# Optimization experiments

Hardware: AMD Instinct MI355X
Metric: run time of the kernel (lower is better)

The kernel has to match this reference:

```python
import jax, jax.numpy as jnp
import numpy as np

S = 8192          # tokens
D = 4096          # model_dim
E = 64            # num_experts
CAP_FACTOR = 1.0
MIN_CAPACITY = 8
CAPACITY = max(int(np.ceil(S / E * CAP_FACTOR)), MIN_CAPACITY)  # = 128


def setup_inputs() -> dict:
    key = jax.random.key(0)
    kx, kw = jax.random.split(key)
    x = jax.random.normal(kx, (S, D), dtype=jnp.float32)
    # torch Linear weight [out_features, in_features] = [E, D]
    wg = jax.random.normal(kw, (E, D), dtype=jnp.float32) * (1.0 / np.sqrt(D))
    return {"x": x, "wg": wg}


def reference(x, wg):
    # logits = wg(input_fp32): [s, e]
    logits = jnp.einsum('sd,ed->se', x.astype(jnp.float32), wg)
    gates = jax.nn.softmax(logits, axis=1)                     # [s, e]

    # top-1 expert per token (argmax of softmax == argmax of logits)
    indices1_s = jnp.argmax(gates, axis=1)                     # [s]
    mask1 = jax.nn.one_hot(indices1_s, E, dtype=jnp.int32)     # [s, e]
    exp_counts = jnp.sum(mask1, axis=0)                        # [e]

    # load-balancing aux loss (uses pre-capacity mask, as in torch)
    me = jnp.mean(gates, axis=0)
    ce = jnp.mean(mask1.astype(jnp.float32), axis=0)
    l_aux = jnp.sum(me * ce) * E

    # capacity truncation: keep first CAPACITY routed tokens per expert
    # (equivalent to mask1 * scatter(topk(mask1, capacity, dim=0)) when
    #  use_rts=False, since topk over 0/1 tie-breaks by lowest index)
    loc0 = jnp.cumsum(mask1, axis=0) - 1                       # [s, e]
    mask1 = mask1 * (loc0 < CAPACITY).astype(jnp.int32)

    # slot positions within each expert's capacity buffer
    locations1 = jnp.cumsum(mask1, axis=0) - 1                 # [s, e]
    locations1_s = jnp.sum(locations1 * mask1, axis=1)         # [s]

    mask1_float = mask1.astype(jnp.float32)
    gates = gates * mask1_float                                # [s, e]
    locations1_sc = jax.nn.one_hot(locations1_s, CAPACITY, dtype=jnp.float32)  # [s, c]

    combine_weights = jnp.einsum('se,sc->sec', gates, locations1_sc)  # [s, e, c]
    dispatch_mask = combine_weights.astype(bool)
    return (l_aux, combine_weights, dispatch_mask, exp_counts)
```

## Files before the change

kernel.cpp:

```cpp
#include <hip/hip_runtime.h>
#include <cstdint>

#define TS 8192
#define TD 4096
#define TE 64
#define TCAP 128
#define KS 8
#define KB (TD/KS)
#define KC 32
#define TB 128
#define NTB (TS/TB)

static constexpr size_t SEC = (size_t)TS * TE * TCAP;

typedef float f32x4 __attribute__((ext_vector_type(4)));

__global__ __launch_bounds__(512, 4) void gemm_fill(
    const float* __restrict__ x, const float* __restrict__ wg,
    float* __restrict__ part, f32x4* __restrict__ out4,
    float* __restrict__ out)
{
    __shared__ float xs[KC][132];
    __shared__ float wsh[KC][68];

    const int tid = threadIdx.x;
    const int bid = blockIdx.x;
    const int tb  = bid & (NTB - 1);
    const int ks  = bid >> 6;
    const int tok0 = tb * TB;
    const int tx = tid & 15;
    const int ty = tid >> 4;
    const int kq_s  = tid & 7;
    const int row_s = tid >> 3;
    const long fill0 = (long)bid * 65536;
    const f32x4 z4 = {0.f, 0.f, 0.f, 0.f};

    float acc[4][4] = {{0,0,0,0},{0,0,0,0},{0,0,0,0},{0,0,0,0}};

    for (int it = 0; it < KB / KC; ++it) {
        const int k0 = ks * KB + it * KC;
        #pragma unroll
        for (int r = 0; r < 2; ++r) {
            const int t = r * 64 + row_s;
            const f32x4 v = __builtin_nontemporal_load(
                reinterpret_cast<const f32x4*>(&x[(size_t)(tok0 + t) * TD + k0 + kq_s * 4]));
            xs[kq_s*4+0][t] = v.x; xs[kq_s*4+1][t] = v.y;
            xs[kq_s*4+2][t] = v.z; xs[kq_s*4+3][t] = v.w;
        }
        {
            const f32x4 v = *reinterpret_cast<const f32x4*>(
                &wg[(size_t)row_s * TD + k0 + kq_s * 4]);
            wsh[kq_s*4+0][row_s] = v.x; wsh[kq_s*4+1][row_s] = v.y;
            wsh[kq_s*4+2][row_s] = v.z; wsh[kq_s*4+3][row_s] = v.w;
        }
        __syncthreads();
        #pragma unroll
        for (int k = 0; k < KC; ++k) {
            if ((k & 3) == 0) {
                const int j = k >> 2;
                __builtin_nontemporal_store(z4,
                    &out4[fill0 + (long)it * 4096 + j * 512 + tid]);
            }
            const f32x4 a = *reinterpret_cast<const f32x4*>(&xs[k][ty * 4]);
            const f32x4 b = *reinterpret_cast<const f32x4*>(&wsh[k][tx * 4]);
            acc[0][0] = fmaf(a.x, b.x, acc[0][0]);
            acc[0][1] = fmaf(a.x, b.y, acc[0][1]);
            acc[0][2] = fmaf(a.x, b.z, acc[0][2]);
            acc[0][3] = fmaf(a.x, b.w, acc[0][3]);
            acc[1][0] = fmaf(a.y, b.x, acc[1][0]);
            acc[1][1] = fmaf(a.y, b.y, acc[1][1]);
            acc[1][2] = fmaf(a.y, b.z, acc[1][2]);
            acc[1][3] = fmaf(a.y, b.w, acc[1][3]);
            acc[2][0] = fmaf(a.z, b.x, acc[2][0]);
            acc[2][1] = fmaf(a.z, b.y, acc[2][1]);
            acc[2][2] = fmaf(a.z, b.z, acc[2][2]);
            acc[2][3] = fmaf(a.z, b.w, acc[2][3]);
            acc[3][0] = fmaf(a.w, b.x, acc[3][0]);
            acc[3][1] = fmaf(a.w, b.y, acc[3][1]);
            acc[3][2] = fmaf(a.w, b.z, acc[3][2]);
            acc[3][3] = fmaf(a.w, b.w, acc[3][3]);
        }
        __syncthreads();
    }
    if (bid == 0 && tid < 65) out[2 * SEC + tid] = 0.f;
    #pragma unroll
    for (int i = 0; i < 4; ++i) {
        const int t = tok0 + ty * 4 + i;
        f32x4 v;
        v.x = acc[i][0]; v.y = acc[i][1]; v.z = acc[i][2]; v.w = acc[i][3];
        *reinterpret_cast<f32x4*>(&part[((size_t)ks * TS + t) * TE + tx * 4]) = v;
    }
}

__global__ __launch_bounds__(256) void softmax_argmax(
    const float* __restrict__ part, int* __restrict__ eidx,
    float* __restrict__ gtop, float* __restrict__ partial_me)
{
    __shared__ float cs[4][64];
    const int tid = threadIdx.x;
    const int tx = tid & 15;
    const int ty = tid >> 4;
    const int s = blockIdx.x * 16 + ty;

    float p[4] = {0.f, 0.f, 0.f, 0.f};
    #pragma unroll
    for (int ks = 0; ks < KS; ++ks) {
        const f32x4 v = *reinterpret_cast<const f32x4*>(
            &part[((size_t)ks * TS + s) * TE + tx * 4]);
        p[0] += v.x; p[1] += v.y; p[2] += v.z; p[3] += v.w;
    }

    float lm = fmaxf(fmaxf(p[0], p[1]), fmaxf(p[2], p[3]));
    #pragma unroll
    for (int mask = 1; mask <= 8; mask <<= 1)
        lm = fmaxf(lm, __shfl_xor(lm, mask));
    float ep[4]; float ls = 0.f;
    #pragma unroll
    for (int j = 0; j < 4; ++j) { ep[j] = __expf(p[j] - lm); ls += ep[j]; }
    #pragma unroll
    for (int mask = 1; mask <= 8; mask <<= 1)
        ls += __shfl_xor(ls, mask);
    const float invZ = 1.0f / ls;

    float bv = p[0]; int bi = tx * 4;
    #pragma unroll
    for (int j = 1; j < 4; ++j)
        if (p[j] > bv) { bv = p[j]; bi = tx * 4 + j; }
    #pragma unroll
    for (int mask = 1; mask <= 8; mask <<= 1) {
        const float ov = __shfl_xor(bv, mask);
        const int   oi = __shfl_xor(bi, mask);
        if (ov > bv || (ov == bv && oi < bi)) { bv = ov; bi = oi; }
    }
    if (tx == 0) { eidx[s] = bi; gtop[s] = invZ; }

    float colsum[4];
    #pragma unroll
    for (int j = 0; j < 4; ++j) colsum[j] = ep[j] * invZ;
    #pragma unroll
    for (int j = 0; j < 4; ++j) {
        colsum[j] += __shfl_xor(colsum[j], 16);
        colsum[j] += __shfl_xor(colsum[j], 32);
    }
    const int wave = tid >> 6;
    const int lane = tid & 63;
    if (lane < 16) {
        #pragma unroll
        for (int j = 0; j < 4; ++j) cs[wave][lane * 4 + j] = colsum[j];
    }
    __syncthreads();
    if (tid < 64) {
        partial_me[(size_t)blockIdx.x * 64 + tid] =
            cs[0][tid] + cs[1][tid] + cs[2][tid] + cs[3][tid];
    }
}

__global__ __launch_bounds__(1024) void rank_scatter_laux(
    const int* __restrict__ eidx, const float* __restrict__ gtop,
    const float* __restrict__ partial_me, float* __restrict__ out)
{
    const int e = blockIdx.x;
    const int tid = threadIdx.x;
    const int wave = tid >> 6;
    const int lane = tid & 63;
    __shared__ int wave_tot[16];
    __shared__ float red[8];

    int ev[8];
    #pragma unroll
    for (int r = 0; r < 8; ++r) ev[r] = eidx[r * 1024 + tid];

    int running = 0;
    #pragma unroll
    for (int r = 0; r < 8; ++r) {
        const bool m = (ev[r] == e);
        const unsigned long long b = __ballot(m);
        if (lane == 0) wave_tot[wave] = __popcll(b);
        __syncthreads();
        int off = running;
        #pragma unroll
        for (int w = 0; w < 16; ++w) if (w < wave) off += wave_tot[w];
        const int rank = off + __popcll(b & ((1ull << lane) - 1ull));
        if (m && rank < TCAP) {
            const int s = r * 1024 + tid;
            const size_t base = 1 + ((size_t)s * TE + e) * TCAP + (size_t)rank;
            out[base] = gtop[s];
            out[base + SEC] = 1.0f;
        }
        int tot = 0;
        #pragma unroll
        for (int w = 0; w < 16; ++w) tot += wave_tot[w];
        running += tot;
        __syncthreads();
    }
    if (tid == 0) out[1 + 2 * SEC + e] = (float)running;

    float v = (tid < 512) ? partial_me[(size_t)tid * 64 + e] : 0.f;
    #pragma unroll
    for (int mask = 32; mask >= 1; mask >>= 1) v += __shfl_xor(v, mask);
    if (lane == 0) { if (wave < 8) red[wave] = v; else if (v != 0.f) red[0] += 0.f; }
    __syncthreads();
    if (tid == 0) {
        float ms = 0.f;
        #pragma unroll
        for (int w = 0; w < 8; ++w) ms += red[w];
        const float me = ms * (1.0f / TS);
        const float ce = (float)running * (1.0f / TS);
        atomicAdd(out, me * ce * (float)TE);
    }
}

extern "C" void kernel_launch(void* const* d_in, const int* in_sizes, int n_in,
                              void* d_out, int out_size, void* d_ws, size_t ws_size,
                              hipStream_t stream) {
    const float* x  = (const float*)d_in[0];
    const float* wg = (const float*)d_in[1];
    float* out = (float*)d_out;

    float* part       = (float*)d_ws;
    int*   eidx       = (int*)(part + (size_t)KS * TS * TE);
    float* gtop       = (float*)(eidx + TS);
    float* partial_me = gtop + TS;
    int*   counts     = (int*)(partial_me + 512 * 64);
    (void)counts;

    hipLaunchKernelGGL(gemm_fill, dim3(512), dim3(512), 0, stream,
                       x, wg, part, (f32x4*)out, out);
    hipLaunchKernelGGL(softmax_argmax, dim3(512), dim3(256), 0, stream,
                       part, eidx, gtop, partial_me);
    hipLaunchKernelGGL(rank_scatter_laux, dim3(64), dim3(1024), 0, stream,
                       eidx, gtop, partial_me, out);
}
```

Measured before the change: 170.2 us.

## Split zero-fill between GEMM blocks and dedicated fill blocks, prefetch next K tile

The fused GEMM kernel now launches 1536 blocks. The first 512 compute partial logits and zero half of the output, and the extra 1024 blocks only stream zeros into the other half. The GEMM loop also register-prefetches the next x/wg tile before computing the current one, so global loads overlap the FMA work. The intent is to spread the large write-bound fill across more CUs and hide load latency. It costs more registers and relies on correct index arithmetic to cover the whole output.

```diff
diff --git a/kernel.cpp b/kernel.cpp
--- a/kernel.cpp
+++ b/kernel.cpp
@@ -15,7 +15,7 @@
 
 typedef float f32x4 __attribute__((ext_vector_type(4)));
 
-__global__ __launch_bounds__(512, 4) void gemm_fill(
+__global__ __launch_bounds__(512, 4) void gemm_fill_fused(
     const float* __restrict__ x, const float* __restrict__ wg,
     float* __restrict__ part, f32x4* __restrict__ out4,
     float* __restrict__ out)
@@ -25,6 +25,22 @@
 
     const int tid = threadIdx.x;
     const int bid = blockIdx.x;
+    const f32x4 z4 = {0.f, 0.f, 0.f, 0.f};
+
+    if (bid >= 512) {
+        const int fid = bid - 512;
+        const long base = 16777216L + (long)fid * 16384;
+        #pragma unroll
+        for (int j = 0; j < 32; ++j)
+            __builtin_nontemporal_store(z4, &out4[base + (long)j * 512 + tid]);
+        if (fid == 0) {
+            if (tid < 16)
+                __builtin_nontemporal_store(z4, &out4[33554432L + tid]);
+            if (tid == 16) out[2 * SEC + 64] = 0.f;
+        }
+        return;
+    }
+
     const int tb  = bid & (NTB - 1);
     const int ks  = bid >> 6;
     const int tok0 = tb * TB;
@@ -32,34 +48,43 @@
     const int ty = tid >> 4;
     const int kq_s  = tid & 7;
     const int row_s = tid >> 3;
-    const long fill0 = (long)bid * 65536;
-    const f32x4 z4 = {0.f, 0.f, 0.f, 0.f};
+    const long fill0 = (long)bid * 32768;
 
     float acc[4][4] = {{0,0,0,0},{0,0,0,0},{0,0,0,0},{0,0,0,0}};
 
+    f32x4 rx[2], rw;
+    {
+        const int k0 = ks * KB;
+        #pragma unroll
+        for (int r = 0; r < 2; ++r)
+            rx[r] = __builtin_nontemporal_load(reinterpret_cast<const f32x4*>(
+                &x[(size_t)(tok0 + r * 64 + row_s) * TD + k0 + kq_s * 4]));
+        rw = *reinterpret_cast<const f32x4*>(&wg[(size_t)row_s * TD + k0 + kq_s * 4]);
+    }
+
     for (int it = 0; it < KB / KC; ++it) {
-        const int k0 = ks * KB + it * KC;
         #pragma unroll
         for (int r = 0; r < 2; ++r) {
             const int t = r * 64 + row_s;
-            const f32x4 v = __builtin_nontemporal_load(
-                reinterpret_cast<const f32x4*>(&x[(size_t)(tok0 + t) * TD + k0 + kq_s * 4]));
-            xs[kq_s*4+0][t] = v.x; xs[kq_s*4+1][t] = v.y;
-            xs[kq_s*4+2][t] = v.z; xs[kq_s*4+3][t] = v.w;
-        }
-        {
-            const f32x4 v = *reinterpret_cast<const f32x4*>(
-                &wg[(size_t)row_s * TD + k0 + kq_s * 4]);
-            wsh[kq_s*4+0][row_s] = v.x; wsh[kq_s*4+1][row_s] = v.y;
-            wsh[kq_s*4+2][row_s] = v.z; wsh[kq_s*4+3][row_s] = v.w;
-        }
-        __syncthreads();
+            xs[kq_s*4+0][t] = rx[r].x; xs[kq_s*4+1][t] = rx[r].y;
+            xs[kq_s*4+2][t] = rx[r].z; xs[kq_s*4+3][t] = rx[r].w;
+        }
+        wsh[kq_s*4+0][row_s] = rw.x; wsh[kq_s*4+1][row_s] = rw.y;
+        wsh[kq_s*4+2][row_s] = rw.z; wsh[kq_s*4+3][row_s] = rw.w;
+        __syncthreads();
+        if (it + 1 < KB / KC) {
+            const int k0 = ks * KB + (it + 1) * KC;
+            #pragma unroll
+            for (int r = 0; r < 2; ++r)
+                rx[r] = __builtin_nontemporal_load(reinterpret_cast<const f32x4*>(
+                    &x[(size_t)(tok0 + r * 64 + row_s) * TD + k0 + kq_s * 4]));
+            rw = *reinterpret_cast<const f32x4*>(&wg[(size_t)row_s * TD + k0 + kq_s * 4]);
+        }
         #pragma unroll
         for (int k = 0; k < KC; ++k) {
-            if ((k & 3) == 0) {
-                const int j = k >> 2;
+            if (k < 4) {
                 __builtin_nontemporal_store(z4,
-                    &out4[fill0 + (long)it * 4096 + j * 512 + tid]);
+                    &out4[fill0 + (long)it * 2048 + k * 512 + tid]);
             }
             const f32x4 a = *reinterpret_cast<const f32x4*>(&xs[k][ty * 4]);
             const f32x4 b = *reinterpret_cast<const f32x4*>(&wsh[k][tx * 4]);
@@ -82,7 +107,6 @@
         }
         __syncthreads();
     }
-    if (bid == 0 && tid < 65) out[2 * SEC + tid] = 0.f;
     #pragma unroll
     for (int i = 0; i < 4; ++i) {
         const int t = tok0 + ty * 4 + i;
@@ -198,7 +222,7 @@
     float v = (tid < 512) ? partial_me[(size_t)tid * 64 + e] : 0.f;
     #pragma unroll
     for (int mask = 32; mask >= 1; mask >>= 1) v += __shfl_xor(v, mask);
-    if (lane == 0) { if (wave < 8) red[wave] = v; else if (v != 0.f) red[0] += 0.f; }
+    if (lane == 0 && wave < 8) red[wave] = v;
     __syncthreads();
     if (tid == 0) {
         float ms = 0.f;
@@ -221,10 +245,8 @@
     int*   eidx       = (int*)(part + (size_t)KS * TS * TE);
     float* gtop       = (float*)(eidx + TS);
     float* partial_me = gtop + TS;
-    int*   counts     = (int*)(partial_me + 512 * 64);
-    (void)counts;
-
-    hipLaunchKernelGGL(gemm_fill, dim3(512), dim3(512), 0, stream,
+
+    hipLaunchKernelGGL(gemm_fill_fused, dim3(1536), dim3(512), 0, stream,
                        x, wg, part, (f32x4*)out, out);
     hipLaunchKernelGGL(softmax_argmax, dim3(512), dim3(256), 0, stream,
                        part, eidx, gtop, partial_me);
```

Result: faster. 149.6 us (-12.1%).
